# Performance work log

Hardware: AMD Instinct MI355X
Metric: run time of the kernel (lower is better)

The kernel has to match this reference:

```python
import jax, jax.numpy as jnp
import numpy as np

D = 256; H = 8; NL = 4; NP = 4; DH = D // H
IMG = 2048; SIDE = 256; NUM_INTERP = 2; PTS = NUM_INTERP + 1
SIDE_LENS = (32, 16, 8, 4)
LEVEL_SHAPES = ((256, 256), (128, 128), (64, 64), (32, 32))
IMG_STARTS = (0, 65536, 81920, 86016)   # level starts in full feature pyramid
VAL_STARTS = (0, 1024, 1280, 1344)      # level starts in cropped pyramid (sum=1360)


def layernorm(x, w, b, eps=1e-5):
    m = x.mean(-1, keepdims=True)
    v = ((x - m) ** 2).mean(-1, keepdims=True)
    return (x - m) * jax.lax.rsqrt(v + eps) * w + b


def pos_encode_2d(x, y, dim=128):
    # DETR-style sinusoidal 2D encoding: 64 dims for y, 64 for x, interleaved sin/cos
    half = dim // 2
    dim_t = 10000.0 ** (2.0 * (jnp.arange(half) // 2) / half)
    def enc(v):
        p = v[..., None] / dim_t
        return jnp.concatenate([jnp.sin(p[..., 0::2])[..., None],
                                jnp.cos(p[..., 1::2])[..., None]], -1).reshape(*v.shape, half)
    return jnp.concatenate([enc(y), enc(x)], -1)


def _forward(mask_flatten, tgt, query_pos, edge_coords, src_flatten, valid_ratios,
             in_proj_w, in_proj_b, out_proj_w, out_proj_b,
             norm1_w, norm1_b, norm2_w, norm2_b, norm3_w, norm3_b,
             lin0_w, lin0_b, lin1_w, lin1_b, lin2_w, lin2_b,
             off_w, off_b, attw_w, attw_b, val_w, val_b, oproj_w, oproj_b):
    E = tgt.shape[1]
    N = E * PTS
    # ---- self attention (dropout = identity, eval mode) ----
    qk = tgt + query_pos
    wq, wk, wv = jnp.split(in_proj_w, 3, 0)
    bq, bk, bv = jnp.split(in_proj_b, 3, 0)
    q = ((qk @ wq.T + bq) * (DH ** -0.5)).reshape(1, E, H, DH)
    k = (qk @ wk.T + bk).reshape(1, E, H, DH)
    v = (tgt @ wv.T + bv).reshape(1, E, H, DH)
    att = jax.nn.softmax(jnp.einsum('behd,bfhd->bhef', q, k), -1)
    sa = jnp.einsum('bhef,bfhd->behd', att, v).reshape(1, E, D) @ out_proj_w.T + out_proj_b
    x = layernorm(tgt + sa, norm2_w, norm2_b)

    # ---- geometry: interp points along edges, crop boxes, segment clipping ----
    a = edge_coords[0, :, :2]
    b = edge_coords[0, :, 2:]
    ts = jnp.arange(PTS, dtype=jnp.float32) / NUM_INTERP
    pts = (a[:, None, :] + ts[None, :, None] * (b - a)[:, None, :]).reshape(N, 2)
    ar = jnp.broadcast_to(a[:, None, :], (E, PTS, 2)).reshape(N, 2)
    br = jnp.broadcast_to(b[:, None, :], (E, PTS, 2)).reshape(N, 2)
    c = jnp.floor(pts).astype(jnp.int32)  # int() truncation, coords > 0
    cx, cy = c[:, 0], c[:, 1]
    minx = jnp.maximum(cx - SIDE // 2, 0)
    minx = jnp.where(minx + SIDE > IMG, IMG - SIDE, minx)
    miny = jnp.maximum(cy - SIDE // 2, 0)
    miny = jnp.where(miny + SIDE > IMG, IMG - SIDE, miny)
    fminx = minx.astype(jnp.float32)
    fminy = miny.astype(jnp.float32)
    d = br - ar
    def axis_clip(p0, d0, lo, hi):
        safe = jnp.where(d0 == 0, 1.0, d0)
        t1 = (lo - p0) / safe
        t2 = (hi - p0) / safe
        tlo = jnp.where(d0 == 0, 0.0, jnp.minimum(t1, t2))
        thi = jnp.where(d0 == 0, 1.0, jnp.maximum(t1, t2))
        return tlo, thi
    tlx, thx = axis_clip(ar[:, 0], d[:, 0], fminx, fminx + SIDE)
    tly, thy = axis_clip(ar[:, 1], d[:, 1], fminy, fminy + SIDE)
    t0 = jnp.maximum(jnp.maximum(tlx, tly), 0.0)
    t1 = jnp.maximum(jnp.minimum(jnp.minimum(thx, thy), 1.0), t0)
    ca = ar + t0[:, None] * d   # clipped segment first endpoint
    cb = ar + t1[:, None] * d   # clipped segment second endpoint
    pos_x = jnp.stack([ca[:, 0], cb[:, 0], cx.astype(jnp.float32)], -1)
    pos_y = jnp.stack([ca[:, 1], cb[:, 1], cy.astype(jnp.float32)], -1)
    pe = pos_encode_2d(pos_x, pos_y).reshape(N, -1)  # [N, 384]

    qfeat = jnp.broadcast_to((x + query_pos)[0][:, None, :], (E, PTS, D)).reshape(N, D)
    nq = jnp.concatenate([qfeat, pe], -1) @ lin0_w.T + lin0_b  # linear0, [N, 256]

    ref = jnp.stack([(cx.astype(jnp.float32) - fminx) / SIDE,
                     (cy.astype(jnp.float32) - fminy) / SIDE], -1)  # [N, 2]
    ref4 = ref[:, None, None, :] * valid_ratios[:, None]  # [N, 1, NL, 2]

    # ---- multi-level feature crops (gather) ----
    srcs, masks = [], []
    for l in range(NL):
        h, w = LEVEL_SHAPES[l]
        s = SIDE_LENS[l]
        ratio = IMG // w
        lx = jnp.round(fminx / ratio).astype(jnp.int32)
        ly = jnp.round(fminy / ratio).astype(jnp.int32)
        rows = ly[:, None] + jnp.arange(s)
        cols = lx[:, None] + jnp.arange(s)
        flat = (rows[:, :, None] * w + cols[:, None, :]).reshape(N, s * s)
        srcs.append(src_flatten[0, IMG_STARTS[l]:IMG_STARTS[l] + h * w][flat])
        masks.append(mask_flatten[0, IMG_STARTS[l]:IMG_STARTS[l] + h * w][flat])
    vsrc = jnp.concatenate(srcs, 1)    # [N, 1360, D]
    vmask = jnp.concatenate(masks, 1)  # [N, 1360]

    # ---- MSDeformAttn cross attention ----
    value = vsrc @ val_w.T + val_b
    value = jnp.where(vmask[..., None], 0.0, value).reshape(N, -1, H, DH)
    off = (nq @ off_w.T + off_b).reshape(N, H, NL, NP, 2)
    aw = jax.nn.softmax((nq @ attw_w.T + attw_b).reshape(N, H, NL * NP), -1).reshape(N, H, NL, NP)
    normalizer = jnp.array([[s, s] for s in SIDE_LENS], jnp.float32)  # (w, h) per crop level
    loc = ref4[:, 0, None, :, None, :] + off / normalizer[None, None, :, None, :]  # [N,H,NL,NP,2]
    n_idx = jnp.arange(N)[:, None, None]
    h_idx = jnp.arange(H)[None, :, None]
    out_acc = jnp.zeros((N, H, DH), jnp.float32)
    for l in range(NL):
        s = SIDE_LENS[l]
        vl = value[:, VAL_STARTS[l]:VAL_STARTS[l] + s * s].reshape(N, s, s, H, DH)
        g = loc[:, :, l]  # [N, H, NP, 2]
        px = g[..., 0] * s - 0.5  # grid_sample align_corners=False
        py = g[..., 1] * s - 0.5
        x0 = jnp.floor(px).astype(jnp.int32)
        y0 = jnp.floor(py).astype(jnp.int32)
        fx = px - x0
        fy = py - y0
        def tap(xi, yi):
            ok = (xi >= 0) & (xi < s) & (yi >= 0) & (yi < s)
            val = vl[n_idx, jnp.clip(yi, 0, s - 1), jnp.clip(xi, 0, s - 1), h_idx]
            return jnp.where(ok[..., None], val, 0.0)
        samp = (tap(x0, y0) * ((1 - fx) * (1 - fy))[..., None]
                + tap(x0 + 1, y0) * (fx * (1 - fy))[..., None]
                + tap(x0, y0 + 1) * ((1 - fx) * fy)[..., None]
                + tap(x0 + 1, y0 + 1) * (fx * fy)[..., None])  # [N,H,NP,DH]
        out_acc = out_acc + (aw[:, :, l, :, None] * samp).sum(2)
    ca_out = out_acc.reshape(N, D) @ oproj_w.T + oproj_b  # [N, D]

    # ---- per-edge mean pooling over interpolation samples ----
    pooled = ca_out.reshape(E, PTS, D).mean(1)[None]
    x = layernorm(x + pooled, norm1_w, norm1_b)
    # ---- FFN ----
    ffn = jax.nn.relu(x @ lin1_w.T + lin1_b) @ lin2_w.T + lin2_b
    return layernorm(x + ffn, norm3_w, norm3_b)


def setup_inputs():
    key = jax.random.key(0)
    ks = jax.random.split(key, 16)
    E = 128
    nrm = lambda k, shape, s=1.0: s * jax.random.normal(k, shape, jnp.float32)
    W = lambda k, o, i: nrm(k, (o, i), 0.02)
    theta = jax.random.uniform(ks[2], (E,), minval=0.0, maxval=2.0 * np.pi)
    start = jax.random.uniform(ks[3], (E, 2), minval=250.0, maxval=1798.0)
    end = start + 200.0 * jnp.stack([jnp.cos(theta), jnp.sin(theta)], -1)  # length 200 -> num_interp=2
    return dict(
        tgt=nrm(ks[0], (1, E, D)),
        query_pos=nrm(ks[1], (1, E, D)),
        edge_coords=jnp.concatenate([start, end], -1)[None],
        src_flatten=nrm(ks[4], (1, 87040, D)),
        mask_flatten=jnp.zeros((1, 87040), bool),
        valid_ratios=jnp.ones((1, 4, 2), jnp.float32),
        in_proj_w=W(ks[5], 3 * D, D), in_proj_b=jnp.zeros(3 * D),
        out_proj_w=W(ks[6], D, D), out_proj_b=jnp.zeros(D),
        norm1_w=jnp.ones(D), norm1_b=jnp.zeros(D),
        norm2_w=jnp.ones(D), norm2_b=jnp.zeros(D),
        norm3_w=jnp.ones(D), norm3_b=jnp.zeros(D),
        lin0_w=W(ks[7], D, 640), lin0_b=jnp.zeros(D),
        lin1_w=W(ks[8], 1024, D), lin1_b=jnp.zeros(1024),
        lin2_w=W(ks[9], D, 1024), lin2_b=jnp.zeros(D),
        off_w=W(ks[10], H * NL * NP * 2, D) * 0.1, off_b=jnp.zeros(H * NL * NP * 2),
        attw_w=W(ks[11], H * NL * NP, D), attw_b=jnp.zeros(H * NL * NP),
        val_w=W(ks[12], D, D), val_b=jnp.zeros(D),
        oproj_w=W(ks[13], D, D), oproj_b=jnp.zeros(D),
    )


def reference(tgt, query_pos, edge_coords, src_flatten, mask_flatten, valid_ratios,
              in_proj_w, in_proj_b, out_proj_w, out_proj_b,
              norm1_w, norm1_b, norm2_w, norm2_b, norm3_w, norm3_b,
              lin0_w, lin0_b, lin1_w, lin1_b, lin2_w, lin2_b,
              off_w, off_b, attw_w, attw_b, val_w, val_b, oproj_w, oproj_b):
    return _forward(mask_flatten, tgt, query_pos, edge_coords, src_flatten, valid_ratios,
                    in_proj_w, in_proj_b, out_proj_w, out_proj_b,
                    norm1_w, norm1_b, norm2_w, norm2_b, norm3_w, norm3_b,
                    lin0_w, lin0_b, lin1_w, lin1_b, lin2_w, lin2_b,
                    off_w, off_b, attw_w, attw_b, val_w, val_b, oproj_w, oproj_b)
```

## Files before the change

kernel.cpp:

```cpp
#include <hip/hip_runtime.h>
#include <math.h>


typedef unsigned int uint;

__device__ __forceinline__ float lo16(uint u) { return __uint_as_float(u << 16); }
__device__ __forceinline__ float hi16(uint u) { return __uint_as_float(u & 0xFFFF0000u); }
__device__ __forceinline__ uint bfr(float x) {
    uint u = __float_as_uint(x);
    return (u + 0x7FFFu + ((u >> 16) & 1u)) >> 16;
}

__device__ __forceinline__ float block_sum256w(float v, float* red) {
    int t = threadIdx.x;
    if (t < 256) red[t] = v;
    __syncthreads();
    for (int st = 128; st > 0; st >>= 1) {
        if (t < st) red[t] += red[t + st];
        __syncthreads();
    }
    float r = red[0]; __syncthreads();
    return r;
}

template <int K, int MI, int MO>
__device__ void gemm_unit(const float* __restrict__ IN, const float* __restrict__ IN2,
                          const float* __restrict__ W, const float* __restrict__ B,
                          float* __restrict__ OUT, int O, int OG, int u, float* smem) {
    constexpr int KC = 128;
    constexpr int LDT = KC + 4;
    float* tile = smem;
    int og = u % OG, rg = u / OG;
    int o0 = og * 8, r0 = rg * 64;
    int t = threadIdx.x;
    int r = t & 63;
    int ol = __builtin_amdgcn_readfirstlane(t >> 6);
    int oa = o0 + ol, ob = o0 + 4 + ol;
    const float* Wa = W + (size_t)oa * K;
    const float* Wb = W + (size_t)ob * K;
    float Ba = B[oa], Bb = B[ob];
    float acca = 0.f, accb = 0.f;
    for (int c = 0; c < K / KC; c++) {
        for (int idx = t; idx < 64 * KC; idx += 256) {
            int rr = idx >> 7, ii = idx & (KC - 1);
            int row = r0 + rr, col = c * KC + ii;
            float v;
            if (MI == 0) {
                v = IN[(size_t)row * K + col];
            } else {
                float tv = IN[row * 256 + col];
                v = (o0 < 512) ? tv + IN2[row * 256 + col] : tv;
            }
            tile[rr * LDT + ii] = v;
        }
        __syncthreads();
        const float4* wa4 = (const float4*)(Wa + c * KC);
        const float4* wb4 = (const float4*)(Wb + c * KC);
        const float4* trow = (const float4*)(tile + r * LDT);
        #pragma unroll
        for (int i4 = 0; i4 < KC / 4; i4++) {
            float4 x4 = trow[i4];
            float4 a4 = wa4[i4];
            float4 b4 = wb4[i4];
            acca += x4.x * a4.x; acca += x4.y * a4.y;
            acca += x4.z * a4.z; acca += x4.w * a4.w;
            accb += x4.x * b4.x; accb += x4.y * b4.y;
            accb += x4.z * b4.z; accb += x4.w * b4.w;
        }
        __syncthreads();
    }
    acca += Ba; accb += Bb;
    if (MO == 2) {
        if (oa < 256) acca *= 0.17677669529663687f;
        if (ob < 256) accb *= 0.17677669529663687f;
    }
    OUT[(size_t)(r0 + r) * O + oa] = acca;
    OUT[(size_t)(r0 + r) * O + ob] = accb;
}

__device__ void transpose_unit(const float* __restrict__ in, float* __restrict__ out,
                               int R, int C, int u, float* smem) {
    int TC = C >> 5;
    int tc = u % TC, tr = u / TC;
    int t = threadIdx.x;
    int lr = t >> 5, lc = t & 31;
    #pragma unroll
    for (int rr = 0; rr < 32; rr += 8)
        smem[(rr + lr) * 33 + lc] = in[(size_t)(tr * 32 + rr + lr) * C + tc * 32 + lc];
    __syncthreads();
    #pragma unroll
    for (int rr = 0; rr < 32; rr += 8)
        out[(size_t)(tc * 32 + rr + lr) * R + tr * 32 + lc] = smem[lc * 33 + rr + lr];
    __syncthreads();
}

__device__ void tpack_unit(const float* __restrict__ in, uint* __restrict__ P,
                           int C, int S, int F, int u, float* smem) {
    int TC = C >> 5;
    int tc = u % TC, tr = u / TC;
    int t = threadIdx.x;
    int lr = t >> 5, lc = t & 31;
    #pragma unroll
    for (int rr = 0; rr < 32; rr += 8)
        smem[(rr + lr) * 33 + lc] = in[(size_t)(tr * 32 + rr + lr) * C + tc * 32 + lc];
    __syncthreads();
    #pragma unroll
    for (int rep = 0; rep < 2; rep++) {
        int idx = rep * 256 + t;
        int c2 = idx >> 5, r = idx & 31;
        uint w0 = bfr(smem[r * 33 + 2 * c2]);
        uint w1 = bfr(smem[r * 33 + 2 * c2 + 1]);
        P[(size_t)(tc * 16 + c2) * S + F + tr * 32 + r] = (w1 << 16) | w0;
    }
    __syncthreads();
}

__global__ __launch_bounds__(256) void k_prep(const float* __restrict__ tgt,
                                              const float* __restrict__ qpos,
                                              const float* __restrict__ ipw,
                                              const float* __restrict__ ipb,
                                              const float* __restrict__ opw,
                                              const float* __restrict__ ojw,
                                              const float* __restrict__ valw,
                                              const float* __restrict__ l1w,
                                              const float* __restrict__ l2w,
                                              const float* __restrict__ l0w,
                                              const float* __restrict__ offw,
                                              const float* __restrict__ aww,
                                              float* __restrict__ qkv,
                                              float* __restrict__ opwT,
                                              float* __restrict__ ojwT,
                                              float* __restrict__ valwT,
                                              uint* __restrict__ Pl1,
                                              uint* __restrict__ Pl2,
                                              uint* __restrict__ Pl0,
                                              uint* __restrict__ Poaw) {
    __shared__ __align__(16) float smem[8448];
    int u = blockIdx.x;
    if (u < 192)       gemm_unit<256, 1, 2>(tgt, qpos, ipw, ipb, qkv, 768, 96, u, smem);
    else if (u < 256)  transpose_unit(opw, opwT, 256, 256, u - 192, smem);
    else if (u < 320)  transpose_unit(ojw, ojwT, 256, 256, u - 256, smem);
    else if (u < 384)  transpose_unit(valw, valwT, 256, 256, u - 320, smem);
    else if (u < 640)  tpack_unit(l1w, Pl1, 256, 1024, 0, u - 384, smem);
    else if (u < 896)  tpack_unit(l2w, Pl2, 1024, 256, 0, u - 640, smem);
    else if (u < 1056) tpack_unit(l0w, Pl0, 640, 256, 0, u - 896, smem);
    else if (u < 1120) tpack_unit(offw, Poaw, 256, 384, 0, u - 1056, smem);
    else               tpack_unit(aww, Poaw, 256, 384, 256, u - 1120, smem);
}

__device__ __forceinline__ void edge_geom(const float* __restrict__ ec, int e, int j,
                                          float* pxs, float* pys,
                                          float& fminx, float& fminy,
                                          float& cxf, float& cyf) {
    float ax = ec[e * 4 + 0], ay = ec[e * 4 + 1];
    float bx = ec[e * 4 + 2], by = ec[e * 4 + 3];
    float dx = bx - ax, dy = by - ay;
    float tj = 0.5f * (float)j;
    float ptx = __fadd_rn(ax, __fmul_rn(tj, dx));
    float pty = __fadd_rn(ay, __fmul_rn(tj, dy));
    cxf = floorf(ptx); cyf = floorf(pty);
    int minx = max((int)cxf - 128, 0); if (minx + 256 > 2048) minx = 2048 - 256;
    int miny = max((int)cyf - 128, 0); if (miny + 256 > 2048) miny = 2048 - 256;
    fminx = (float)minx; fminy = (float)miny;
    float tlx, thx, tly, thy;
    if (dx == 0.f) { tlx = 0.f; thx = 1.f; }
    else { float u1 = (fminx - ax) / dx, u2 = (fminx + 256.f - ax) / dx; tlx = fminf(u1, u2); thx = fmaxf(u1, u2); }
    if (dy == 0.f) { tly = 0.f; thy = 1.f; }
    else { float u1 = (fminy - ay) / dy, u2 = (fminy + 256.f - ay) / dy; tly = fminf(u1, u2); thy = fmaxf(u1, u2); }
    float t0 = fmaxf(fmaxf(tlx, tly), 0.f);
    float t1 = fmaxf(fminf(fminf(thx, thy), 1.f), t0);
    pxs[0] = __fadd_rn(ax, __fmul_rn(t0, dx)); pys[0] = __fadd_rn(ay, __fmul_rn(t0, dy));
    pxs[1] = __fadd_rn(ax, __fmul_rn(t1, dx)); pys[1] = __fadd_rn(ay, __fmul_rn(t1, dy));
    pxs[2] = cxf; pys[2] = cyf;
}

__global__ __launch_bounds__(1024) void k_edge(const float* __restrict__ qkv,
                                               const float* __restrict__ tgt,
                                               const float* __restrict__ qpos,
                                               const float* __restrict__ opwT,
                                               const float* __restrict__ opb,
                                               const float* __restrict__ n2w,
                                               const float* __restrict__ n2b,
                                               const float* __restrict__ ec,
                                               const uint* __restrict__ Pl0,
                                               const float* __restrict__ l0b,
                                               const uint* __restrict__ Poaw,
                                               const float* __restrict__ offb,
                                               const float* __restrict__ awb,
                                               float* __restrict__ x1,
                                               float* __restrict__ offatr,
                                               float* __restrict__ refxy,
                                               int* __restrict__ lxly) {
    int n = blockIdx.x, t = threadIdx.x;
    int e = n / 3, j = n - e * 3;
    __shared__ __align__(16) float SH[14208];
    float* xq   = SH;
    float* sq   = SH + 256;
    float* sS   = SH + 512;
    float* smax = SH + 1536;
    float* ssum = SH + 1544;
    float* srow = SH + 1552;
    float* part = SH + 1808;
    float* red  = SH + 2832;
    float* pe    = SH + 256;
    float* nrow  = SH + 640;
    float* partial = SH + 896;
    uint*  wt    = (uint*)(SH + 1920);
    if (t < 256) sq[t] = qkv[e * 768 + t];
    __syncthreads();
    {
        int h = t >> 7, f = t & 127;
        const float* kf = qkv + f * 768 + 256 + h * 32;
        const float* qh = sq + h * 32;
        float s = 0.f;
        #pragma unroll 8
        for (int d = 0; d < 32; d++) s += qh[d] * kf[d];
        sS[t] = s;
    }
    __syncthreads();
    if (t < 8) {
        float m = -1e30f;
        for (int f = 0; f < 128; f++) m = fmaxf(m, sS[t * 128 + f]);
        smax[t] = m;
    }
    __syncthreads();
    sS[t] = __expf(sS[t] - smax[t >> 7]);
    __syncthreads();
    if (t < 8) {
        float s = 0.f;
        for (int f = 0; f < 128; f++) s += sS[t * 128 + f];
        ssum[t] = 1.f / s;
    }
    __syncthreads();
    {
        int o = t & 255, c = t >> 8, h = o >> 5, d = o & 31;
        float acc = 0.f;
        #pragma unroll 8
        for (int f = c * 32; f < c * 32 + 32; f++)
            acc += sS[h * 128 + f] * qkv[f * 768 + 512 + h * 32 + d];
        part[t] = acc;
    }
    __syncthreads();
    if (t < 256) srow[t] = (part[t] + part[256 + t] + part[512 + t] + part[768 + t]) * ssum[t >> 5];
    __syncthreads();
    {
        int o = t & 255, c = t >> 8;
        float acc = 0.f;
        #pragma unroll 8
        for (int i = c * 64; i < c * 64 + 64; i++) acc += srow[i] * opwT[(size_t)i * 256 + o];
        part[t] = acc;
    }
    __syncthreads();
    {
        float acc = 0.f;
        if (t < 256) acc = part[t] + part[256 + t] + part[512 + t] + part[768 + t] + opb[t] + tgt[e * 256 + t];
        float mean = block_sum256w(acc, red) * (1.f / 256.f);
        float d0 = acc - mean;
        float var = block_sum256w((t < 256) ? d0 * d0 : 0.f, red) * (1.f / 256.f);
        if (t < 256) {
            float xln = d0 * rsqrtf(var + 1e-5f) * n2w[t] + n2b[t];
            if (j == 0) x1[e * 256 + t] = xln;
            xq[t] = xln + qpos[e * 256 + t];
        }
    }
    if (t < 384) {
        float pxs[3], pys[3], fmx, fmy, cxf, cyf;
        edge_geom(ec, e, j, pxs, pys, fmx, fmy, cxf, cyf);
        int jj = t >> 7, tt = t & 127, i = tt & 63, kk = i >> 1;
        float invd = __expf(-(float)kk * (9.210340371976184f / 32.f));
        float vv = (tt < 64) ? pys[jj] : pxs[jj];
        float pp = vv * invd;
        pe[t] = (i & 1) ? __cosf(pp) : __sinf(pp);
    }
    if (t == 0) {
        float pxs[3], pys[3], fmx, fmy, cxf, cyf;
        edge_geom(ec, e, j, pxs, pys, fmx, fmy, cxf, cyf);
        refxy[n * 2 + 0] = (cxf - fmx) * (1.f / 256.f);
        refxy[n * 2 + 1] = (cyf - fmy) * (1.f / 256.f);
        lxly[n * 8 + 0] = (int)rintf(fmx * 0.125f);
        lxly[n * 8 + 1] = (int)rintf(fmx * 0.0625f);
        lxly[n * 8 + 2] = (int)rintf(fmx * 0.03125f);
        lxly[n * 8 + 3] = (int)rintf(fmx * 0.015625f);
        lxly[n * 8 + 4] = (int)rintf(fmy * 0.125f);
        lxly[n * 8 + 5] = (int)rintf(fmy * 0.0625f);
        lxly[n * 8 + 6] = (int)rintf(fmy * 0.03125f);
        lxly[n * 8 + 7] = (int)rintf(fmy * 0.015625f);
    }
    __syncthreads();
    {
        int o = t & 255, kc = t >> 8;
        float acc = 0.f;
        for (int tk = 0; tk < 10; tk++) {
            const uint4* s4 = (const uint4*)(Pl0 + (size_t)tk * 8192);
            uint4* d4 = (uint4*)wt;
            d4[t] = s4[t];
            d4[1024 + t] = s4[1024 + t];
            __syncthreads();
            const float* inb = (tk < 4) ? (xq + tk * 64) : (pe + tk * 64 - 256);
            #pragma unroll
            for (int kk = 0; kk < 8; kk++) {
                uint u = wt[(kc * 8 + kk) * 256 + o];
                acc += inb[(kc * 8 + kk) * 2] * lo16(u);
                acc += inb[(kc * 8 + kk) * 2 + 1] * hi16(u);
            }
            __syncthreads();
        }
        partial[t] = acc;
    }
    __syncthreads();
    if (t < 256) nrow[t] = partial[t] + partial[256 + t] + partial[512 + t] + partial[768 + t] + l0b[t];
    __syncthreads();
    {
        int o = t % 384, kc = t / 384;
        float acc = 0.f;
        for (int tk = 0; tk < 4; tk++) {
            const uint4* s4 = (const uint4*)(Poaw + (size_t)tk * 12288);
            uint4* d4 = (uint4*)wt;
            d4[t] = s4[t];
            d4[1024 + t] = s4[1024 + t];
            d4[2048 + t] = s4[2048 + t];
            __syncthreads();
            if (t < 768) {
                const float* inb = nrow + tk * 64 + kc * 32;
                #pragma unroll
                for (int kk = 0; kk < 16; kk++) {
                    uint u = wt[(kc * 16 + kk) * 384 + o];
                    acc += inb[kk * 2] * lo16(u);
                    acc += inb[kk * 2 + 1] * hi16(u);
                }
            }
            __syncthreads();
        }
        if (t < 768) partial[t] = acc;
    }
    __syncthreads();
    if (t < 384) {
        float b = (t < 256) ? offb[t] : awb[t - 256];
        offatr[(size_t)n * 384 + t] = partial[t] + partial[384 + t] + b;
    }
}

__global__ __launch_bounds__(1024) void k_sample(const float* __restrict__ offatr,
                                                 const float* __restrict__ refxy,
                                                 const float* __restrict__ vr,
                                                 const int* __restrict__ lxly,
                                                 const float* __restrict__ src,
                                                 const unsigned char* __restrict__ mask,
                                                 const float* __restrict__ valwT,
                                                 const float* __restrict__ valb,
                                                 float* __restrict__ ca) {
    int n = blockIdx.x, t = threadIdx.x;
    __shared__ float sl[128];
    __shared__ float sm[8], sinv[8];
    __shared__ float sw[512];
    __shared__ int   sg[512];
    __shared__ int   lead[512];
    __shared__ int   rk[512];
    __shared__ int   ulist[512];
    __shared__ int   redi[256];
    __shared__ float uw[512 * 8];
    __shared__ float agg[8 * 256];
    __shared__ float pcs[64];
    __shared__ float pagg[1024];

    if (t < 128) sl[t] = offatr[(size_t)n * 384 + 256 + t];
    #pragma unroll
    for (int z = 0; z < 4; z++) uw[z * 1024 + t] = 0.f;
    __syncthreads();
    if (t < 8) {
        float m = -1e30f;
        for (int i = 0; i < 16; i++) m = fmaxf(m, sl[t * 16 + i]);
        float s = 0.f;
        for (int i = 0; i < 16; i++) s += __expf(sl[t * 16 + i] - m);
        sm[t] = m; sinv[t] = 1.f / s;
    }
    __syncthreads();
    if (t < 512) {
        int h = t >> 6, r = t & 63;
        int l = r >> 4, pp = (r >> 2) & 3, tap = r & 3;
        int s = 32 >> l, wl = 256 >> l;
        const int img_starts[4] = {0, 65536, 81920, 86016};
        float a = __expf(sl[h * 16 + l * 4 + pp] - sm[h]) * sinv[h];
        float slv = (float)s;
        float gx = refxy[n * 2 + 0] * vr[l * 2 + 0] + offatr[(size_t)n * 384 + h * 32 + l * 8 + pp * 2 + 0] / slv;
        float gy = refxy[n * 2 + 1] * vr[l * 2 + 1] + offatr[(size_t)n * 384 + h * 32 + l * 8 + pp * 2 + 1] / slv;
        float px = gx * slv - 0.5f, py = gy * slv - 0.5f;
        float x0 = floorf(px), y0 = floorf(py);
        float fx = px - x0, fy = py - y0;
        int xi = (int)x0 + (tap & 1), yi = (int)y0 + (tap >> 1);
        float wtt = ((tap & 1) ? fx : (1.f - fx)) * ((tap >> 1) ? fy : (1.f - fy));
        int g = -1;
        if (xi >= 0 && xi < s && yi >= 0 && yi < s) {
            int col = lxly[n * 8 + l] + xi;
            int row = lxly[n * 8 + 4 + l] + yi;
            g = img_starts[l] + row * wl + col;
            if (mask[g]) g = -1;
        }
        sw[t] = a * wtt;
        sg[t] = g;
    }
    __syncthreads();
    int fi = -1;
    if (t < 512) {
        int g = sg[t];
        if (g >= 0) {
            fi = t;
            for (int jj = 0; jj < t; jj++) if (sg[jj] == g) { fi = jj; break; }
        }
        lead[t] = (fi == t) ? 1 : 0;
    }
    __syncthreads();
    if (t < 512 && fi == t) {
        int r = 0;
        for (int jj = 0; jj < t; jj++) r += lead[jj];
        rk[t] = r;
        ulist[r] = sg[t];
    }
    if (t < 256) redi[t] = lead[t] + lead[t + 256];
    __syncthreads();
    for (int st = 128; st > 0; st >>= 1) {
        if (t < st) redi[t] += redi[t + st];
        __syncthreads();
    }
    if (t < 512 && fi >= 0) {
        int h = t >> 6;
        atomicAdd(&uw[rk[fi] * 8 + h], sw[t]);
    }
    __syncthreads();
    int U = redi[0];
    {
        int ch = t & 255, q = t >> 8;
        float a0 = 0.f, a1 = 0.f;
        for (int u = 0; u < U; u++) {
            int g = ulist[u];
            float v = src[(size_t)g * 256 + ch];
            a0 += uw[u * 8 + 2 * q] * v;
            a1 += uw[u * 8 + 2 * q + 1] * v;
        }
        agg[(2 * q) * 256 + ch] = a0;
        agg[(2 * q + 1) * 256 + ch] = a1;
    }
    if (t < 64) {
        int h = t >> 3, p = t & 7;
        float s = 0.f;
        for (int u = p; u < U; u += 8) s += uw[u * 8 + h];
        pcs[t] = s;
    }
    __syncthreads();
    {
        int h = t >> 7, rem = t & 127, o = rem & 31, kc = rem >> 5;
        const float* ag = agg + h * 256 + kc * 64;
        const float* w = valwT + (size_t)(kc * 64) * 256 + h * 32 + o;
        float pv = 0.f;
        #pragma unroll 8
        for (int i = 0; i < 64; i++) pv += ag[i] * w[(size_t)i * 256];
        pagg[t] = pv;
    }
    __syncthreads();
    if (t < 256) {
        int h = t >> 5, o = t & 31;
        float cs = pcs[h * 8 + 0] + pcs[h * 8 + 1] + pcs[h * 8 + 2] + pcs[h * 8 + 3]
                 + pcs[h * 8 + 4] + pcs[h * 8 + 5] + pcs[h * 8 + 6] + pcs[h * 8 + 7];
        float r = pagg[h * 128 + o] + pagg[h * 128 + 32 + o] + pagg[h * 128 + 64 + o] + pagg[h * 128 + 96 + o];
        ca[(size_t)n * 256 + h * 32 + o] = r + cs * valb[h * 32 + o];
    }
}

__global__ __launch_bounds__(1024) void k_tail(const float* __restrict__ ca,
                                               const float* __restrict__ x1,
                                               const float* __restrict__ ojwT,
                                               const float* __restrict__ ojb,
                                               const float* __restrict__ n1w,
                                               const float* __restrict__ n1b,
                                               const uint* __restrict__ Pl1,
                                               const float* __restrict__ l1b,
                                               const uint* __restrict__ Pl2,
                                               const float* __restrict__ l2b,
                                               const float* __restrict__ n3w,
                                               const float* __restrict__ n3b,
                                               float* __restrict__ out) {
    int e = blockIdx.x, t = threadIdx.x;
    __shared__ float row[256], red[256], x2s[256], h1s[1024], part[1024];
    if (t < 256)
        row[t] = (ca[(3 * e) * 256 + t] + ca[(3 * e + 1) * 256 + t] + ca[(3 * e + 2) * 256 + t]) * (1.f / 3.f);
    __syncthreads();
    {
        int o = t & 255, c = t >> 8;
        float acc = 0.f;
        #pragma unroll 8
        for (int i = c * 64; i < c * 64 + 64; i++) acc += row[i] * ojwT[(size_t)i * 256 + o];
        part[t] = acc;
    }
    __syncthreads();
    {
        float acc = 0.f;
        if (t < 256) acc = part[t] + part[256 + t] + part[512 + t] + part[768 + t] + ojb[t] + x1[e * 256 + t];
        float mean = block_sum256w(acc, red) * (1.f / 256.f);
        float d0 = acc - mean;
        float var = block_sum256w((t < 256) ? d0 * d0 : 0.f, red) * (1.f / 256.f);
        if (t < 256) x2s[t] = d0 * rsqrtf(var + 1e-5f) * n1w[t] + n1b[t];
    }
    __syncthreads();
    {
        float acc = l1b[t];
        #pragma unroll 8
        for (int k2 = 0; k2 < 128; k2++) {
            uint u = Pl1[(size_t)k2 * 1024 + t];
            acc += x2s[2 * k2] * lo16(u);
            acc += x2s[2 * k2 + 1] * hi16(u);
        }
        h1s[t] = fmaxf(acc, 0.f);
    }
    __syncthreads();
    {
        int o = t & 255, c = t >> 8;
        float acc = 0.f;
        #pragma unroll 8
        for (int k2 = c * 128; k2 < c * 128 + 128; k2++) {
            uint u = Pl2[(size_t)k2 * 256 + o];
            acc += h1s[2 * k2] * lo16(u);
            acc += h1s[2 * k2 + 1] * hi16(u);
        }
        part[t] = acc;
    }
    __syncthreads();
    {
        float acc = 0.f;
        if (t < 256) acc = part[t] + part[256 + t] + part[512 + t] + part[768 + t] + l2b[t] + x2s[t];
        float mean = block_sum256w(acc, red) * (1.f / 256.f);
        float d0 = acc - mean;
        float var = block_sum256w((t < 256) ? d0 * d0 : 0.f, red) * (1.f / 256.f);
        if (t < 256) out[e * 256 + t] = d0 * rsqrtf(var + 1e-5f) * n3w[t] + n3b[t];
    }
}

extern "C" void kernel_launch(void* const* d_in, const int* in_sizes, int n_in,
                              void* d_out, int out_size, void* d_ws, size_t ws_size,
                              hipStream_t stream) {
    (void)in_sizes; (void)n_in; (void)out_size; (void)ws_size;
    const float* tgt  = (const float*)d_in[0];
    const float* qpos = (const float*)d_in[1];
    const float* ec   = (const float*)d_in[2];
    const float* src  = (const float*)d_in[3];
    const unsigned char* mask = (const unsigned char*)d_in[4];
    const float* vr   = (const float*)d_in[5];
    const float* ipw  = (const float*)d_in[6];
    const float* ipb  = (const float*)d_in[7];
    const float* opw  = (const float*)d_in[8];
    const float* opb  = (const float*)d_in[9];
    const float* n1w  = (const float*)d_in[10];
    const float* n1b  = (const float*)d_in[11];
    const float* n2w  = (const float*)d_in[12];
    const float* n2b  = (const float*)d_in[13];
    const float* n3w  = (const float*)d_in[14];
    const float* n3b  = (const float*)d_in[15];
    const float* l0w  = (const float*)d_in[16];
    const float* l0b  = (const float*)d_in[17];
    const float* l1w  = (const float*)d_in[18];
    const float* l1b  = (const float*)d_in[19];
    const float* l2w  = (const float*)d_in[20];
    const float* l2b  = (const float*)d_in[21];
    const float* offw = (const float*)d_in[22];
    const float* offb = (const float*)d_in[23];
    const float* aww  = (const float*)d_in[24];
    const float* awb  = (const float*)d_in[25];
    const float* valw = (const float*)d_in[26];
    const float* valb = (const float*)d_in[27];
    const float* ojw  = (const float*)d_in[28];
    const float* ojb  = (const float*)d_in[29];

    float* ws     = (float*)d_ws;
    float* qkv    = ws;
    float* x1     = ws + 98304;
    float* offatr = ws + 131072;
    float* ca     = ws + 278528;
    float* refxy  = ws + 376832;
    int*   lxly   = (int*)(ws + 377600);
    float* opwT   = ws + 380672;
    float* ojwT   = ws + 446208;
    float* valwT  = ws + 511744;
    uint*  Pl1    = (uint*)(ws + 577280);
    uint*  Pl2    = (uint*)(ws + 708352);
    uint*  Pl0    = (uint*)(ws + 839424);
    uint*  Poaw   = (uint*)(ws + 921344);

    k_prep<<<1152, 256, 0, stream>>>(tgt, qpos, ipw, ipb, opw, ojw, valw, l1w, l2w,
                                     l0w, offw, aww,
                                     qkv, opwT, ojwT, valwT, Pl1, Pl2, Pl0, Poaw);
    k_edge<<<384, 1024, 0, stream>>>(qkv, tgt, qpos, opwT, opb, n2w, n2b, ec,
                                     Pl0, l0b, Poaw, offb, awb,
                                     x1, offatr, refxy, lxly);
    k_sample<<<384, 1024, 0, stream>>>(offatr, refxy, vr, lxly, src, mask, valwT, valb, ca);
    k_tail<<<128, 1024, 0, stream>>>(ca, x1, ojwT, ojb, n1w, n1b, Pl1, l1b, Pl2, l2b, n3w, n3b, (float*)d_out);
}
```

Before: 277.2 us.

## Split per-point linears out of edge kernel into batched tiled GEMM kernels

Self-attention now runs once per edge (128 blocks) instead of redundantly for each of the three points per edge. The lin0 and offset/attention-weight projections move into separate batched fp32 GEMM kernels that read the original weights directly, so those weights no longer need bf16 packing in the prep kernel. In k_sample, the sampling tasks are reordered level-major and duplicate detection only scans within a level. The cost is two extra kernel launches and intermediate buffers in global memory, and those linears now use fp32 weights instead of bf16.

```diff
diff --git a/kernel.cpp b/kernel.cpp
--- a/kernel.cpp
+++ b/kernel.cpp
@@ -124,17 +124,12 @@
                                               const float* __restrict__ valw,
                                               const float* __restrict__ l1w,
                                               const float* __restrict__ l2w,
-                                              const float* __restrict__ l0w,
-                                              const float* __restrict__ offw,
-                                              const float* __restrict__ aww,
                                               float* __restrict__ qkv,
                                               float* __restrict__ opwT,
                                               float* __restrict__ ojwT,
                                               float* __restrict__ valwT,
                                               uint* __restrict__ Pl1,
-                                              uint* __restrict__ Pl2,
-                                              uint* __restrict__ Pl0,
-                                              uint* __restrict__ Poaw) {
+                                              uint* __restrict__ Pl2) {
     __shared__ __align__(16) float smem[8448];
     int u = blockIdx.x;
     if (u < 192)       gemm_unit<256, 1, 2>(tgt, qpos, ipw, ipb, qkv, 768, 96, u, smem);
@@ -142,10 +137,7 @@
     else if (u < 320)  transpose_unit(ojw, ojwT, 256, 256, u - 256, smem);
     else if (u < 384)  transpose_unit(valw, valwT, 256, 256, u - 320, smem);
     else if (u < 640)  tpack_unit(l1w, Pl1, 256, 1024, 0, u - 384, smem);
-    else if (u < 896)  tpack_unit(l2w, Pl2, 1024, 256, 0, u - 640, smem);
-    else if (u < 1056) tpack_unit(l0w, Pl0, 640, 256, 0, u - 896, smem);
-    else if (u < 1120) tpack_unit(offw, Poaw, 256, 384, 0, u - 1056, smem);
-    else               tpack_unit(aww, Poaw, 256, 384, 256, u - 1120, smem);
+    else               tpack_unit(l2w, Pl2, 1024, 256, 0, u - 640, smem);
 }
 
 __device__ __forceinline__ void edge_geom(const float* __restrict__ ec, int e, int j,
@@ -174,7 +166,7 @@
     pxs[2] = cxf; pys[2] = cyf;
 }
 
-__global__ __launch_bounds__(1024) void k_edge(const float* __restrict__ qkv,
+__global__ __launch_bounds__(1024) void k_attn(const float* __restrict__ qkv,
                                                const float* __restrict__ tgt,
                                                const float* __restrict__ qpos,
                                                const float* __restrict__ opwT,
@@ -182,30 +174,19 @@
                                                const float* __restrict__ n2w,
                                                const float* __restrict__ n2b,
                                                const float* __restrict__ ec,
-                                               const uint* __restrict__ Pl0,
-                                               const float* __restrict__ l0b,
-                                               const uint* __restrict__ Poaw,
-                                               const float* __restrict__ offb,
-                                               const float* __restrict__ awb,
                                                float* __restrict__ x1,
-                                               float* __restrict__ offatr,
+                                               float* __restrict__ nqin,
                                                float* __restrict__ refxy,
                                                int* __restrict__ lxly) {
-    int n = blockIdx.x, t = threadIdx.x;
-    int e = n / 3, j = n - e * 3;
-    __shared__ __align__(16) float SH[14208];
-    float* xq   = SH;
-    float* sq   = SH + 256;
-    float* sS   = SH + 512;
-    float* smax = SH + 1536;
-    float* ssum = SH + 1544;
-    float* srow = SH + 1552;
-    float* part = SH + 1808;
-    float* red  = SH + 2832;
-    float* pe    = SH + 256;
-    float* nrow  = SH + 640;
-    float* partial = SH + 896;
-    uint*  wt    = (uint*)(SH + 1920);
+    int e = blockIdx.x, t = threadIdx.x;
+    __shared__ __align__(16) float SH[2832];
+    float* sq   = SH;
+    float* sS   = SH + 256;
+    float* smax = SH + 1280;
+    float* ssum = SH + 1288;
+    float* srow = SH + 1296;
+    float* part = SH + 1552;
+    float* red  = SH + 2576;
     if (t < 256) sq[t] = qkv[e * 768 + t];
     __syncthreads();
     {
@@ -259,22 +240,27 @@
         float var = block_sum256w((t < 256) ? d0 * d0 : 0.f, red) * (1.f / 256.f);
         if (t < 256) {
             float xln = d0 * rsqrtf(var + 1e-5f) * n2w[t] + n2b[t];
-            if (j == 0) x1[e * 256 + t] = xln;
-            xq[t] = xln + qpos[e * 256 + t];
-        }
-    }
-    if (t < 384) {
+            x1[e * 256 + t] = xln;
+            float xqv = xln + qpos[e * 256 + t];
+            nqin[(size_t)(3 * e + 0) * 640 + t] = xqv;
+            nqin[(size_t)(3 * e + 1) * 640 + t] = xqv;
+            nqin[(size_t)(3 * e + 2) * 640 + t] = xqv;
+        }
+    }
+    for (int idx = t; idx < 1152; idx += 1024) {
+        int j = idx / 384, w = idx - j * 384;
         float pxs[3], pys[3], fmx, fmy, cxf, cyf;
         edge_geom(ec, e, j, pxs, pys, fmx, fmy, cxf, cyf);
-        int jj = t >> 7, tt = t & 127, i = tt & 63, kk = i >> 1;
+        int jj = w >> 7, tt = w & 127, i = tt & 63, kk = i >> 1;
         float invd = __expf(-(float)kk * (9.210340371976184f / 32.f));
         float vv = (tt < 64) ? pys[jj] : pxs[jj];
         float pp = vv * invd;
-        pe[t] = (i & 1) ? __cosf(pp) : __sinf(pp);
-    }
-    if (t == 0) {
+        nqin[(size_t)(3 * e + j) * 640 + 256 + w] = (i & 1) ? __cosf(pp) : __sinf(pp);
+    }
+    if (t < 3) {
+        int n = 3 * e + t;
         float pxs[3], pys[3], fmx, fmy, cxf, cyf;
-        edge_geom(ec, e, j, pxs, pys, fmx, fmy, cxf, cyf);
+        edge_geom(ec, e, t, pxs, pys, fmx, fmy, cxf, cyf);
         refxy[n * 2 + 0] = (cxf - fmx) * (1.f / 256.f);
         refxy[n * 2 + 1] = (cyf - fmy) * (1.f / 256.f);
         lxly[n * 8 + 0] = (int)rintf(fmx * 0.125f);
@@ -286,58 +272,54 @@
         lxly[n * 8 + 6] = (int)rintf(fmy * 0.03125f);
         lxly[n * 8 + 7] = (int)rintf(fmy * 0.015625f);
     }
-    __syncthreads();
-    {
-        int o = t & 255, kc = t >> 8;
-        float acc = 0.f;
-        for (int tk = 0; tk < 10; tk++) {
-            const uint4* s4 = (const uint4*)(Pl0 + (size_t)tk * 8192);
-            uint4* d4 = (uint4*)wt;
-            d4[t] = s4[t];
-            d4[1024 + t] = s4[1024 + t];
-            __syncthreads();
-            const float* inb = (tk < 4) ? (xq + tk * 64) : (pe + tk * 64 - 256);
-            #pragma unroll
-            for (int kk = 0; kk < 8; kk++) {
-                uint u = wt[(kc * 8 + kk) * 256 + o];
-                acc += inb[(kc * 8 + kk) * 2] * lo16(u);
-                acc += inb[(kc * 8 + kk) * 2 + 1] * hi16(u);
-            }
-            __syncthreads();
-        }
-        partial[t] = acc;
-    }
-    __syncthreads();
-    if (t < 256) nrow[t] = partial[t] + partial[256 + t] + partial[512 + t] + partial[768 + t] + l0b[t];
-    __syncthreads();
-    {
-        int o = t % 384, kc = t / 384;
-        float acc = 0.f;
-        for (int tk = 0; tk < 4; tk++) {
-            const uint4* s4 = (const uint4*)(Poaw + (size_t)tk * 12288);
-            uint4* d4 = (uint4*)wt;
-            d4[t] = s4[t];
-            d4[1024 + t] = s4[1024 + t];
-            d4[2048 + t] = s4[2048 + t];
-            __syncthreads();
-            if (t < 768) {
-                const float* inb = nrow + tk * 64 + kc * 32;
-                #pragma unroll
-                for (int kk = 0; kk < 16; kk++) {
-                    uint u = wt[(kc * 16 + kk) * 384 + o];
-                    acc += inb[kk * 2] * lo16(u);
-                    acc += inb[kk * 2 + 1] * hi16(u);
-                }
-            }
-            __syncthreads();
-        }
-        if (t < 768) partial[t] = acc;
-    }
-    __syncthreads();
-    if (t < 384) {
-        float b = (t < 256) ? offb[t] : awb[t - 256];
-        offatr[(size_t)n * 384 + t] = partial[t] + partial[384 + t] + b;
-    }
+}
+
+template <int K>
+__global__ __launch_bounds__(256) void k_lin(const float* __restrict__ IN,
+                                             const float* __restrict__ W1,
+                                             const float* __restrict__ B1,
+                                             const float* __restrict__ W2,
+                                             const float* __restrict__ B2,
+                                             float* __restrict__ OUT,
+                                             int out_stride, int OG) {
+    constexpr int KC = 128;
+    constexpr int LDT = KC + 4;
+    __shared__ __align__(16) float tile[64 * LDT];
+    int u = blockIdx.x;
+    int og = u % OG, rg = u / OG;
+    int o0 = og * 8, r0 = rg * 64;
+    int t = threadIdx.x;
+    int r = t & 63;
+    int ol = __builtin_amdgcn_readfirstlane(t >> 6);
+    int oa = o0 + ol, ob = o0 + 4 + ol;
+    const float* Wa = (oa < 256) ? W1 + (size_t)oa * K : W2 + (size_t)(oa - 256) * K;
+    const float* Wb = (ob < 256) ? W1 + (size_t)ob * K : W2 + (size_t)(ob - 256) * K;
+    float Ba = (oa < 256) ? B1[oa] : B2[oa - 256];
+    float Bb = (ob < 256) ? B1[ob] : B2[ob - 256];
+    float acca = 0.f, accb = 0.f;
+    for (int c = 0; c < K / KC; c++) {
+        for (int idx = t; idx < 64 * KC; idx += 256) {
+            int rr = idx >> 7, ii = idx & (KC - 1);
+            tile[rr * LDT + ii] = IN[(size_t)(r0 + rr) * K + c * KC + ii];
+        }
+        __syncthreads();
+        const float4* wa4 = (const float4*)(Wa + c * KC);
+        const float4* wb4 = (const float4*)(Wb + c * KC);
+        const float4* trow = (const float4*)(tile + r * LDT);
+        #pragma unroll
+        for (int i4 = 0; i4 < KC / 4; i4++) {
+            float4 x4 = trow[i4];
+            float4 a4 = wa4[i4];
+            float4 b4 = wb4[i4];
+            acca += x4.x * a4.x; acca += x4.y * a4.y;
+            acca += x4.z * a4.z; acca += x4.w * a4.w;
+            accb += x4.x * b4.x; accb += x4.y * b4.y;
+            accb += x4.z * b4.z; accb += x4.w * b4.w;
+        }
+        __syncthreads();
+    }
+    OUT[(size_t)(r0 + r) * out_stride + oa] = acca + Ba;
+    OUT[(size_t)(r0 + r) * out_stride + ob] = accb + Bb;
 }
 
 __global__ __launch_bounds__(1024) void k_sample(const float* __restrict__ offatr,
@@ -376,8 +358,8 @@
     }
     __syncthreads();
     if (t < 512) {
-        int h = t >> 6, r = t & 63;
-        int l = r >> 4, pp = (r >> 2) & 3, tap = r & 3;
+        int l = t >> 7, rem = t & 127;
+        int h = rem >> 4, pp = (rem >> 2) & 3, tap = t & 3;
         int s = 32 >> l, wl = 256 >> l;
         const int img_starts[4] = {0, 65536, 81920, 86016};
         float a = __expf(sl[h * 16 + l * 4 + pp] - sm[h]) * sinv[h];
@@ -405,7 +387,8 @@
         int g = sg[t];
         if (g >= 0) {
             fi = t;
-            for (int jj = 0; jj < t; jj++) if (sg[jj] == g) { fi = jj; break; }
+            int base = t & ~127;
+            for (int jj = base; jj < t; jj++) if (sg[jj] == g) { fi = jj; break; }
         }
         lead[t] = (fi == t) ? 1 : 0;
     }
@@ -423,7 +406,7 @@
         __syncthreads();
     }
     if (t < 512 && fi >= 0) {
-        int h = t >> 6;
+        int h = (t >> 4) & 7;
         atomicAdd(&uw[rk[fi] * 8 + h], sw[t]);
     }
     __syncthreads();
@@ -581,15 +564,15 @@
     float* valwT  = ws + 511744;
     uint*  Pl1    = (uint*)(ws + 577280);
     uint*  Pl2    = (uint*)(ws + 708352);
-    uint*  Pl0    = (uint*)(ws + 839424);
-    uint*  Poaw   = (uint*)(ws + 921344);
-
-    k_prep<<<1152, 256, 0, stream>>>(tgt, qpos, ipw, ipb, opw, ojw, valw, l1w, l2w,
-                                     l0w, offw, aww,
-                                     qkv, opwT, ojwT, valwT, Pl1, Pl2, Pl0, Poaw);
-    k_edge<<<384, 1024, 0, stream>>>(qkv, tgt, qpos, opwT, opb, n2w, n2b, ec,
-                                     Pl0, l0b, Poaw, offb, awb,
-                                     x1, offatr, refxy, lxly);
+    float* nqin   = ws + 839424;
+    float* nrow   = ws + 1085184;
+
+    k_prep<<<896, 256, 0, stream>>>(tgt, qpos, ipw, ipb, opw, ojw, valw, l1w, l2w,
+                                    qkv, opwT, ojwT, valwT, Pl1, Pl2);
+    k_attn<<<128, 1024, 0, stream>>>(qkv, tgt, qpos, opwT, opb, n2w, n2b, ec,
+                                     x1, nqin, refxy, lxly);
+    k_lin<640><<<192, 256, 0, stream>>>(nqin, l0w, l0b, l0w, l0b, nrow, 256, 32);
+    k_lin<256><<<288, 256, 0, stream>>>(nrow, offw, offb, aww, awb, offatr, 384, 48);
     k_sample<<<384, 1024, 0, stream>>>(offatr, refxy, vr, lxly, src, mask, valwT, valb, ca);
     k_tail<<<128, 1024, 0, stream>>>(ca, x1, ojwT, ojb, n1w, n1b, Pl1, l1b, Pl2, l2b, n3w, n3b, (float*)d_out);
 }
```

Result: slower. 303.3 us (+9.4%).

## Prefetch next weight tile into registers and regroup sampling taps by level

Applied to the files above, without the earlier changes.

The two GEMV loops now load the next weight tile from global memory into registers while the current tile in shared memory is being consumed. This overlaps global-load latency with compute, at the cost of extra registers per thread. The sampling-tap thread mapping is also reordered so taps are grouped by pyramid level rather than by head. Since identical gather indices can only occur within the same level, the duplicate-search scan is limited to that level's 128-entry block, which cuts the quadratic dedup loop.

```diff
diff --git a/kernel.cpp b/kernel.cpp
--- a/kernel.cpp
+++ b/kernel.cpp
@@ -290,12 +290,17 @@
     {
         int o = t & 255, kc = t >> 8;
         float acc = 0.f;
+        uint4* d4 = (uint4*)wt;
+        const uint4* s4 = (const uint4*)Pl0;
+        uint4 pA = s4[t], pB = s4[1024 + t];
         for (int tk = 0; tk < 10; tk++) {
-            const uint4* s4 = (const uint4*)(Pl0 + (size_t)tk * 8192);
-            uint4* d4 = (uint4*)wt;
-            d4[t] = s4[t];
-            d4[1024 + t] = s4[1024 + t];
+            d4[t] = pA;
+            d4[1024 + t] = pB;
             __syncthreads();
+            if (tk < 9) {
+                const uint4* nx = (const uint4*)(Pl0 + (size_t)(tk + 1) * 8192);
+                pA = nx[t]; pB = nx[1024 + t];
+            }
             const float* inb = (tk < 4) ? (xq + tk * 64) : (pe + tk * 64 - 256);
             #pragma unroll
             for (int kk = 0; kk < 8; kk++) {
@@ -313,13 +318,18 @@
     {
         int o = t % 384, kc = t / 384;
         float acc = 0.f;
+        uint4* d4 = (uint4*)wt;
+        const uint4* s4 = (const uint4*)Poaw;
+        uint4 pA = s4[t], pB = s4[1024 + t], pC = s4[2048 + t];
         for (int tk = 0; tk < 4; tk++) {
-            const uint4* s4 = (const uint4*)(Poaw + (size_t)tk * 12288);
-            uint4* d4 = (uint4*)wt;
-            d4[t] = s4[t];
-            d4[1024 + t] = s4[1024 + t];
-            d4[2048 + t] = s4[2048 + t];
+            d4[t] = pA;
+            d4[1024 + t] = pB;
+            d4[2048 + t] = pC;
             __syncthreads();
+            if (tk < 3) {
+                const uint4* nx = (const uint4*)(Poaw + (size_t)(tk + 1) * 12288);
+                pA = nx[t]; pB = nx[1024 + t]; pC = nx[2048 + t];
+            }
             if (t < 768) {
                 const float* inb = nrow + tk * 64 + kc * 32;
                 #pragma unroll
@@ -376,8 +386,8 @@
     }
     __syncthreads();
     if (t < 512) {
-        int h = t >> 6, r = t & 63;
-        int l = r >> 4, pp = (r >> 2) & 3, tap = r & 3;
+        int l = t >> 7, rem = t & 127;
+        int h = rem >> 4, pp = (rem >> 2) & 3, tap = t & 3;
         int s = 32 >> l, wl = 256 >> l;
         const int img_starts[4] = {0, 65536, 81920, 86016};
         float a = __expf(sl[h * 16 + l * 4 + pp] - sm[h]) * sinv[h];
@@ -405,7 +415,8 @@
         int g = sg[t];
         if (g >= 0) {
             fi = t;
-            for (int jj = 0; jj < t; jj++) if (sg[jj] == g) { fi = jj; break; }
+            int base = t & ~127;
+            for (int jj = base; jj < t; jj++) if (sg[jj] == g) { fi = jj; break; }
         }
         lead[t] = (fi == t) ? 1 : 0;
     }
@@ -423,7 +434,7 @@
         __syncthreads();
     }
     if (t < 512 && fi >= 0) {
-        int h = t >> 6;
+        int h = (t >> 4) & 7;
         atomicAdd(&uw[rk[fi] * 8 + h], sw[t]);
     }
     __syncthreads();
```

Result: no change. 275.8 us (-0.5%).

## Replace shared-memory tree reductions with wave shuffles and ballot-based compaction

Applied to the files above, without the earlier changes.

Block sums and the softmax max/sum now use wavefront shuffle-xor reductions plus a small per-wave array, instead of log-step shared-memory trees with a barrier per step. The linear layers for lin0 and offset/attention weights read bf16-packed weights straight from global memory instead of staging tiles in LDS with barriers, which also shrinks the shared footprint. In the sampling kernel, the sample-to-level index mapping is reordered so duplicate-gather detection only scans within a 128-wide level segment, and leader ranks come from ballot/popcount prefix sums instead of serial scans and a tree reduction. The cost is less weight reuse through LDS and more reliance on the cache for repeated global weight reads.

```diff
diff --git a/kernel.cpp b/kernel.cpp
--- a/kernel.cpp
+++ b/kernel.cpp
@@ -11,16 +11,14 @@
     return (u + 0x7FFFu + ((u >> 16) & 1u)) >> 16;
 }
 
-__device__ __forceinline__ float block_sum256w(float v, float* red) {
+__device__ __forceinline__ float block_sum256f(float v, float* red) {
     int t = threadIdx.x;
-    if (t < 256) red[t] = v;
-    __syncthreads();
-    for (int st = 128; st > 0; st >>= 1) {
-        if (t < st) red[t] += red[t + st];
-        __syncthreads();
-    }
-    float r = red[0]; __syncthreads();
-    return r;
+    __syncthreads();
+    #pragma unroll
+    for (int off = 32; off; off >>= 1) v += __shfl_xor(v, off);
+    if (t < 256 && (t & 63) == 0) red[t >> 6] = v;
+    __syncthreads();
+    return red[0] + red[1] + red[2] + red[3];
 }
 
 template <int K, int MI, int MO>
@@ -193,51 +191,49 @@
                                                int* __restrict__ lxly) {
     int n = blockIdx.x, t = threadIdx.x;
     int e = n / 3, j = n - e * 3;
-    __shared__ __align__(16) float SH[14208];
+    __shared__ __align__(16) float SH[2880];
     float* xq   = SH;
     float* sq   = SH + 256;
     float* sS   = SH + 512;
-    float* smax = SH + 1536;
-    float* ssum = SH + 1544;
-    float* srow = SH + 1552;
-    float* part = SH + 1808;
-    float* red  = SH + 2832;
-    float* pe    = SH + 256;
-    float* nrow  = SH + 640;
+    float* wred = SH + 1536;
+    float* ssum = SH + 1552;
+    float* srow = SH + 1560;
+    float* part = SH + 1824;
+    float* red  = SH + 2848;
+    float* pe      = SH + 256;
+    float* nrow    = SH + 640;
     float* partial = SH + 896;
-    uint*  wt    = (uint*)(SH + 1920);
     if (t < 256) sq[t] = qkv[e * 768 + t];
     __syncthreads();
-    {
-        int h = t >> 7, f = t & 127;
+    int h = t >> 7;
+    {
+        int f = t & 127;
         const float* kf = qkv + f * 768 + 256 + h * 32;
         const float* qh = sq + h * 32;
         float s = 0.f;
         #pragma unroll 8
         for (int d = 0; d < 32; d++) s += qh[d] * kf[d];
-        sS[t] = s;
-    }
-    __syncthreads();
-    if (t < 8) {
-        float m = -1e30f;
-        for (int f = 0; f < 128; f++) m = fmaxf(m, sS[t * 128 + f]);
-        smax[t] = m;
-    }
-    __syncthreads();
-    sS[t] = __expf(sS[t] - smax[t >> 7]);
-    __syncthreads();
-    if (t < 8) {
-        float s = 0.f;
-        for (int f = 0; f < 128; f++) s += sS[t * 128 + f];
-        ssum[t] = 1.f / s;
-    }
-    __syncthreads();
-    {
-        int o = t & 255, c = t >> 8, h = o >> 5, d = o & 31;
+        float m = s;
+        #pragma unroll
+        for (int off = 32; off; off >>= 1) m = fmaxf(m, __shfl_xor(m, off));
+        if ((t & 63) == 0) wred[t >> 6] = m;
+        __syncthreads();
+        float hm = fmaxf(wred[2 * h], wred[2 * h + 1]);
+        float ev = __expf(s - hm);
+        sS[t] = ev;
+        float su = ev;
+        #pragma unroll
+        for (int off = 32; off; off >>= 1) su += __shfl_xor(su, off);
+        if ((t & 63) == 0) wred[t >> 6] = su;
+        __syncthreads();
+        if (t < 8) ssum[t] = 1.f / (wred[2 * t] + wred[2 * t + 1]);
+    }
+    {
+        int o = t & 255, c = t >> 8, hh = o >> 5, d = o & 31;
         float acc = 0.f;
         #pragma unroll 8
         for (int f = c * 32; f < c * 32 + 32; f++)
-            acc += sS[h * 128 + f] * qkv[f * 768 + 512 + h * 32 + d];
+            acc += sS[hh * 128 + f] * qkv[f * 768 + 512 + hh * 32 + d];
         part[t] = acc;
     }
     __syncthreads();
@@ -254,9 +250,9 @@
     {
         float acc = 0.f;
         if (t < 256) acc = part[t] + part[256 + t] + part[512 + t] + part[768 + t] + opb[t] + tgt[e * 256 + t];
-        float mean = block_sum256w(acc, red) * (1.f / 256.f);
+        float mean = block_sum256f(acc, red) * (1.f / 256.f);
         float d0 = acc - mean;
-        float var = block_sum256w((t < 256) ? d0 * d0 : 0.f, red) * (1.f / 256.f);
+        float var = block_sum256f((t < 256) ? d0 * d0 : 0.f, red) * (1.f / 256.f);
         if (t < 256) {
             float xln = d0 * rsqrtf(var + 1e-5f) * n2w[t] + n2b[t];
             if (j == 0) x1[e * 256 + t] = xln;
@@ -291,47 +287,34 @@
         int o = t & 255, kc = t >> 8;
         float acc = 0.f;
         for (int tk = 0; tk < 10; tk++) {
-            const uint4* s4 = (const uint4*)(Pl0 + (size_t)tk * 8192);
-            uint4* d4 = (uint4*)wt;
-            d4[t] = s4[t];
-            d4[1024 + t] = s4[1024 + t];
-            __syncthreads();
             const float* inb = (tk < 4) ? (xq + tk * 64) : (pe + tk * 64 - 256);
+            const uint* P = Pl0 + (size_t)tk * 8192 + (size_t)(kc * 8) * 256 + o;
             #pragma unroll
             for (int kk = 0; kk < 8; kk++) {
-                uint u = wt[(kc * 8 + kk) * 256 + o];
+                uint u = P[kk * 256];
                 acc += inb[(kc * 8 + kk) * 2] * lo16(u);
                 acc += inb[(kc * 8 + kk) * 2 + 1] * hi16(u);
             }
-            __syncthreads();
         }
         partial[t] = acc;
     }
     __syncthreads();
     if (t < 256) nrow[t] = partial[t] + partial[256 + t] + partial[512 + t] + partial[768 + t] + l0b[t];
     __syncthreads();
-    {
+    if (t < 768) {
         int o = t % 384, kc = t / 384;
         float acc = 0.f;
         for (int tk = 0; tk < 4; tk++) {
-            const uint4* s4 = (const uint4*)(Poaw + (size_t)tk * 12288);
-            uint4* d4 = (uint4*)wt;
-            d4[t] = s4[t];
-            d4[1024 + t] = s4[1024 + t];
-            d4[2048 + t] = s4[2048 + t];
-            __syncthreads();
-            if (t < 768) {
-                const float* inb = nrow + tk * 64 + kc * 32;
-                #pragma unroll
-                for (int kk = 0; kk < 16; kk++) {
-                    uint u = wt[(kc * 16 + kk) * 384 + o];
-                    acc += inb[kk * 2] * lo16(u);
-                    acc += inb[kk * 2 + 1] * hi16(u);
-                }
+            const float* inb = nrow + tk * 64 + kc * 32;
+            const uint* P = Poaw + (size_t)tk * 12288 + (size_t)(kc * 16) * 384 + o;
+            #pragma unroll
+            for (int kk = 0; kk < 16; kk++) {
+                uint u = P[kk * 384];
+                acc += inb[kk * 2] * lo16(u);
+                acc += inb[kk * 2 + 1] * hi16(u);
             }
-            __syncthreads();
-        }
-        if (t < 768) partial[t] = acc;
+        }
+        partial[t] = acc;
     }
     __syncthreads();
     if (t < 384) {
@@ -354,10 +337,9 @@
     __shared__ float sm[8], sinv[8];
     __shared__ float sw[512];
     __shared__ int   sg[512];
-    __shared__ int   lead[512];
     __shared__ int   rk[512];
     __shared__ int   ulist[512];
-    __shared__ int   redi[256];
+    __shared__ int   wtot[16];
     __shared__ float uw[512 * 8];
     __shared__ float agg[8 * 256];
     __shared__ float pcs[64];
@@ -376,8 +358,8 @@
     }
     __syncthreads();
     if (t < 512) {
-        int h = t >> 6, r = t & 63;
-        int l = r >> 4, pp = (r >> 2) & 3, tap = r & 3;
+        int l = t >> 7, rem = t & 127;
+        int h = rem >> 4, pp = (rem >> 2) & 3, tap = t & 3;
         int s = 32 >> l, wl = 256 >> l;
         const int img_starts[4] = {0, 65536, 81920, 86016};
         float a = __expf(sl[h * 16 + l * 4 + pp] - sm[h]) * sinv[h];
@@ -405,29 +387,33 @@
         int g = sg[t];
         if (g >= 0) {
             fi = t;
-            for (int jj = 0; jj < t; jj++) if (sg[jj] == g) { fi = jj; break; }
-        }
-        lead[t] = (fi == t) ? 1 : 0;
-    }
-    __syncthreads();
-    if (t < 512 && fi == t) {
-        int r = 0;
-        for (int jj = 0; jj < t; jj++) r += lead[jj];
+            int base = t & ~127;
+            for (int jj = base; jj < t; jj++) if (sg[jj] == g) { fi = jj; break; }
+        }
+    }
+    bool islead = (fi == t);
+    unsigned long long bal = __ballot(islead);
+    int lane = t & 63, wid = t >> 6;
+    if ((t & 63) == 0) wtot[wid] = __popcll(bal);
+    __syncthreads();
+    int woff = 0, U = 0;
+    #pragma unroll
+    for (int w = 0; w < 8; w++) {
+        int c = wtot[w];
+        if (w < wid) woff += c;
+        U += c;
+    }
+    if (islead) {
+        int r = woff + __popcll(bal & ((1ULL << lane) - 1ULL));
         rk[t] = r;
         ulist[r] = sg[t];
     }
-    if (t < 256) redi[t] = lead[t] + lead[t + 256];
-    __syncthreads();
-    for (int st = 128; st > 0; st >>= 1) {
-        if (t < st) redi[t] += redi[t + st];
-        __syncthreads();
-    }
-    if (t < 512 && fi >= 0) {
-        int h = t >> 6;
+    __syncthreads();
+    if (fi >= 0) {
+        int h = (t >> 4) & 7;
         atomicAdd(&uw[rk[fi] * 8 + h], sw[t]);
     }
     __syncthreads();
-    int U = redi[0];
     {
         int ch = t & 255, q = t >> 8;
         float a0 = 0.f, a1 = 0.f;
@@ -480,7 +466,7 @@
                                                const float* __restrict__ n3b,
                                                float* __restrict__ out) {
     int e = blockIdx.x, t = threadIdx.x;
-    __shared__ float row[256], red[256], x2s[256], h1s[1024], part[1024];
+    __shared__ float row[256], red[8], x2s[256], h1s[1024], part[1024];
     if (t < 256)
         row[t] = (ca[(3 * e) * 256 + t] + ca[(3 * e + 1) * 256 + t] + ca[(3 * e + 2) * 256 + t]) * (1.f / 3.f);
     __syncthreads();
@@ -495,9 +481,9 @@
     {
         float acc = 0.f;
         if (t < 256) acc = part[t] + part[256 + t] + part[512 + t] + part[768 + t] + ojb[t] + x1[e * 256 + t];
-        float mean = block_sum256w(acc, red) * (1.f / 256.f);
+        float mean = block_sum256f(acc, red) * (1.f / 256.f);
         float d0 = acc - mean;
-        float var = block_sum256w((t < 256) ? d0 * d0 : 0.f, red) * (1.f / 256.f);
+        float var = block_sum256f((t < 256) ? d0 * d0 : 0.f, red) * (1.f / 256.f);
         if (t < 256) x2s[t] = d0 * rsqrtf(var + 1e-5f) * n1w[t] + n1b[t];
     }
     __syncthreads();
@@ -527,9 +513,9 @@
     {
         float acc = 0.f;
         if (t < 256) acc = part[t] + part[256 + t] + part[512 + t] + part[768 + t] + l2b[t] + x2s[t];
-        float mean = block_sum256w(acc, red) * (1.f / 256.f);
+        float mean = block_sum256f(acc, red) * (1.f / 256.f);
         float d0 = acc - mean;
-        float var = block_sum256w((t < 256) ? d0 * d0 : 0.f, red) * (1.f / 256.f);
+        float var = block_sum256f((t < 256) ? d0 * d0 : 0.f, red) * (1.f / 256.f);
         if (t < 256) out[e * 256 + t] = d0 * rsqrtf(var + 1e-5f) * n3w[t] + n3b[t];
     }
 }
```

Result: faster. 264.5 us (median of 2 runs) (-4.6%).
